# Kernel tuning notes

Measured on AMD Instinct MI355X. Metric: run time of the kernel, lower is better.

The kernel has to match this reference:

```python
import jax, jax.numpy as jnp
import numpy as np

V, D, NH, L, HID, E, K = 32000, 1024, 16, 2, 2048, 8, 2
B, S = 2, 1024
HD = D // NH
EPS = 1e-6
ROPE_BASE = 10000.0


def setup_inputs() -> dict:
    key = jax.random.key(0)
    ks = jax.random.split(key, 12)
    s = 0.02
    return {
        "tokens": jax.random.randint(ks[0], (B, S), 0, V),
        "embed": jax.random.normal(ks[1], (V, D), jnp.float32) * s,
        "attn_norm_w": jnp.ones((L, D), jnp.float32),
        "wq": jax.random.normal(ks[2], (L, D, D), jnp.float32) * s,
        "wk": jax.random.normal(ks[3], (L, D, D), jnp.float32) * s,
        "wv": jax.random.normal(ks[4], (L, D, D), jnp.float32) * s,
        "wo": jax.random.normal(ks[5], (L, D, D), jnp.float32) * s,
        "moe_norm_w": jnp.ones((L, D), jnp.float32),
        "router_w": jax.random.normal(ks[6], (L, E, D), jnp.float32) * s,
        "w1": jax.random.normal(ks[7], (L, E, D, HID), jnp.float32) * s,
        "w2": jax.random.normal(ks[8], (L, E, HID, D), jnp.float32) * s,
        "w3": jax.random.normal(ks[9], (L, E, D, HID), jnp.float32) * s,
        "final_norm_w": jnp.ones((D,), jnp.float32),
    }


def rmsnorm(x, w):
    var = jnp.mean(jnp.square(x), axis=-1, keepdims=True)
    return x * jax.lax.rsqrt(var + EPS) * w


def rope(x):  # x: [B, S, NH, HD], rotate-half convention
    half = HD // 2
    inv = ROPE_BASE ** (-jnp.arange(half, dtype=jnp.float32) / half)
    ang = jnp.arange(x.shape[1], dtype=jnp.float32)[:, None] * inv[None, :]  # [S, half]
    cos = jnp.cos(ang)[None, :, None, :]
    sin = jnp.sin(ang)[None, :, None, :]
    x1, x2 = x[..., :half], x[..., half:]
    return jnp.concatenate([x1 * cos - x2 * sin, x1 * sin + x2 * cos], axis=-1)


def attention(x, wq, wk, wv, wo):
    q = (x @ wq).reshape(B, S, NH, HD)
    k = (x @ wk).reshape(B, S, NH, HD)
    v = (x @ wv).reshape(B, S, NH, HD)
    q, k = rope(q), rope(k)
    scores = jnp.einsum("bqhd,bkhd->bhqk", q, k) / jnp.sqrt(jnp.float32(HD))
    mask = jnp.tril(jnp.ones((S, S), bool))
    scores = jnp.where(mask[None, None], scores, jnp.finfo(scores.dtype).min)
    attn = jax.nn.softmax(scores, axis=-1)
    ctx = jnp.einsum("bhqk,bkhd->bqhd", attn, v).reshape(B, S, D)
    return ctx @ wo


def moe(x, router_w, w1, w2, w3):
    flat = x.reshape(-1, D)                      # [T, D]
    T = flat.shape[0]
    logits = flat @ router_w.T                   # [T, E]
    topv, topi = jax.lax.top_k(logits, K)
    topw = jax.nn.softmax(topv, axis=-1)         # softmax over selected logits
    gates = jnp.zeros((T, E), flat.dtype).at[jnp.arange(T)[:, None], topi].set(topw)
    out = jnp.zeros_like(flat)
    for e in range(E):  # small fixed expert count; gates are exact-sparse so math == dispatch path
        y = (jax.nn.silu(flat @ w1[e]) * (flat @ w3[e])) @ w2[e]
        out = out + y * gates[:, e:e + 1]
    return out.reshape(x.shape)


def reference(tokens, embed, attn_norm_w, wq, wk, wv, wo, moe_norm_w,
              router_w, w1, w2, w3, final_norm_w):
    x = embed[tokens]  # [B, S, D]
    for l in range(L):
        x = x + attention(rmsnorm(x, attn_norm_w[l]), wq[l], wk[l], wv[l], wo[l])
        x = x + moe(rmsnorm(x, moe_norm_w[l]), router_w[l], w1[l], w2[l], w3[l])
    x = rmsnorm(x, final_norm_w)
    return x @ embed.T  # tied logits [B, S, V]
```

## Files before the change

kernel.cpp:

```cpp
#include <hip/hip_runtime.h>
#include <math.h>

typedef unsigned short u16;
typedef unsigned int u32;
typedef __attribute__((ext_vector_type(8))) short bf16x8;
typedef __attribute__((ext_vector_type(4))) float f32x4;

#define TOK 2048
#define SEQ 1024
#define DM 1024
#define NEXP 8
#define VOCAB 32000
#define NL 2
#define SLOTS 5120
#define APAD 40

__device__ __forceinline__ float bf2f(u16 v) {
  u32 u = ((u32)v) << 16; float f; __builtin_memcpy(&f, &u, 4); return f;
}
__device__ __forceinline__ u16 f2bf(float f) {
  u32 u; __builtin_memcpy(&u, &f, 4);
  u += 0x7fffu + ((u >> 16) & 1u);
  return (u16)(u >> 16);
}
// ... 45 lines not shown
  ((ushort4*)(ohi + (long)t * DM))[threadIdx.x] = hi;
  ((ushort4*)(olo + (long)t * DM))[threadIdx.x] = lo;
}

__global__ __launch_bounds__(256) void k_rmsnorm_b(const float* __restrict__ x,
    const float* __restrict__ w, u16* __restrict__ out) {
  int t = blockIdx.x;
  float4 v = ((const float4*)(x + (long)t * DM))[threadIdx.x];
  float ss = v.x * v.x + v.y * v.y + v.z * v.z + v.w * v.w;
  for (int off = 32; off; off >>= 1) ss += __shfl_xor(ss, off);
  __shared__ float red[4];
  if ((threadIdx.x & 63) == 0) red[threadIdx.x >> 6] = ss;
  __syncthreads();
  float tot = red[0] + red[1] + red[2] + red[3];
  float sc = rsqrtf(tot * (1.0f / 1024.0f) + 1e-6f);
  float4 wv = ((const float4*)w)[threadIdx.x];
  ushort4 o;
  o.x = f2bf(v.x * sc * wv.x); o.y = f2bf(v.y * sc * wv.y);
  o.z = f2bf(v.z * sc * wv.z); o.w = f2bf(v.w * sc * wv.w);
  ((ushort4*)(out + (long)t * DM))[threadIdx.x] = o;
}

#define KP 72
#define VP 40
#define PP 36
__global__ __launch_bounds__(256) void k_attn(const float* __restrict__ qkv,
    u16* __restrict__ chi, u16* __restrict__ clo) {
  __shared__ u16 Ksh[32 * KP], Ksl[32 * KP];
  __shared__ u16 Vsh[64 * VP], Vsl[64 * VP];
  __shared__ float Ps[4][16 * PP];
  int bid = blockIdx.x;
  int xcd = bid & 7, r = bid >> 3;
  int bh = xcd * 4 + (r >> 4);
  int qt = r & 15;
  int b = bh >> 4, h = bh & 15;
  int tid = threadIdx.x, w = tid >> 6, lane = tid & 63;
  int lrow = lane & 15, lgrp = lane >> 4;
  int q0 = qt * 64;
  long qrow = (long)(b * SEQ + q0 + w * 16 + lrow);
  bf16x8 qh[2], ql[2];
#pragma unroll
  for (int dsl = 0; dsl < 2; dsl++) {
    const float* src = qkv + qrow * 3072 + h * 64 + dsl * 32 + lgrp * 8;
    float v[8];
    *(float4*)v = *(const float4*)src;
    *(float4*)(v + 4) = *(const float4*)(src + 4);
    u16 hi[8], lo[8];
    split8(v, hi, lo);
    qh[dsl] = *(bf16x8*)hi; ql[dsl] = *(bf16x8*)lo;
  }
  f32x4 cacc[4] = {};
  float mst[4], lst[4];
#pragma unroll
  for (int j = 0; j < 4; j++) { mst[j] = -__builtin_inff(); lst[j] = 0.0f; }
  int srow = tid >> 3, dchunk = (tid & 7) * 8;
  for (int s0 = 0; s0 < q0 + 64; s0 += 32) {
    long kvrow = (long)(b * SEQ + s0 + srow) * 3072 + h * 64;
    {
      const float* ksrc = qkv + kvrow + 1024 + dchunk;
      float v[8];
      *(float4*)v = *(const float4*)ksrc;
      *(float4*)(v + 4) = *(const float4*)(ksrc + 4);
#pragma unroll
      for (int j = 0; j < 8; j++) {
        u16 hi = f2bf(v[j]);
        Ksh[srow * KP + dchunk + j] = hi;
        Ksl[srow * KP + dchunk + j] = f2bf(v[j] - bf2f(hi));
      }
      const float* vsrc = qkv + kvrow + 2048 + dchunk;
      *(float4*)v = *(const float4*)vsrc;
      *(float4*)(v + 4) = *(const float4*)(vsrc + 4);
#pragma unroll
      for (int j = 0; j < 8; j++) {
        u16 hi = f2bf(v[j]);
        Vsh[(dchunk + j) * VP + srow] = hi;
        Vsl[(dchunk + j) * VP + srow] = f2bf(v[j] - bf2f(hi));
      }
    }
    __syncthreads();
    f32x4 sacc[2] = {};
#pragma unroll
    for (int sf = 0; sf < 2; sf++)
#pragma unroll
      for (int dsl = 0; dsl < 2; dsl++) {
        bf16x8 kh = *(const bf16x8*)(Ksh + (sf * 16 + lrow) * KP + dsl * 32 + lgrp * 8);
        bf16x8 kl = *(const bf16x8*)(Ksl + (sf * 16 + lrow) * KP + dsl * 32 + lgrp * 8);
        sacc[sf] = __builtin_amdgcn_mfma_f32_16x16x32_bf16(qh[dsl], kh, sacc[sf], 0, 0, 0);
        sacc[sf] = __builtin_amdgcn_mfma_f32_16x16x32_bf16(qh[dsl], kl, sacc[sf], 0, 0, 0);
        sacc[sf] = __builtin_amdgcn_mfma_f32_16x16x32_bf16(ql[dsl], kh, sacc[sf], 0, 0, 0);
      }
#pragma unroll
    for (int sf = 0; sf < 2; sf++)
#pragma unroll
      for (int j = 0; j < 4; j++) {
        int col = s0 + sf * 16 + lrow;
        int row = q0 + w * 16 + lgrp * 4 + j;
        float v = sacc[sf][j] * 0.125f;
        sacc[sf][j] = (col <= row) ? v : -1e30f;
      }
    float fac[4];
#pragma unroll
    for (int j = 0; j < 4; j++) {
      float mx = fmaxf(sacc[0][j], sacc[1][j]);
      for (int off = 1; off < 16; off <<= 1) mx = fmaxf(mx, __shfl_xor(mx, off));
      float mnew = fmaxf(mst[j], mx);
      float f = __expf(mst[j] - mnew);
      mst[j] = mnew;
      float p0 = __expf(sacc[0][j] - mnew);
      float p1 = __expf(sacc[1][j] - mnew);
      sacc[0][j] = p0; sacc[1][j] = p1;
      float ps = p0 + p1;
      for (int off = 1; off < 16; off <<= 1) ps += __shfl_xor(ps, off);
      lst[j] = lst[j] * f + ps;
      fac[j] = f;
    }
#pragma unroll
    for (int n = 0; n < 4; n++)
#pragma unroll
      for (int j = 0; j < 4; j++) cacc[n][j] *= fac[j];
#pragma unroll
    for (int sf = 0; sf < 2; sf++)
#pragma unroll
      for (int j = 0; j < 4; j++)
        Ps[w][(lgrp * 4 + j) * PP + sf * 16 + lrow] = sacc[sf][j];
    float pv[8];
#pragma unroll
    for (int j = 0; j < 8; j++) pv[j] = Ps[w][lrow * PP + lgrp * 8 + j];
    u16 phi[8], plo[8];
    split8(pv, phi, plo);
    bf16x8 ph = *(bf16x8*)phi, pl = *(bf16x8*)plo;
#pragma unroll
    for (int n = 0; n < 4; n++) {
      bf16x8 vh = *(const bf16x8*)(Vsh + (n * 16 + lrow) * VP + lgrp * 8);
      bf16x8 vl = *(const bf16x8*)(Vsl + (n * 16 + lrow) * VP + lgrp * 8);
      cacc[n] = __builtin_amdgcn_mfma_f32_16x16x32_bf16(ph, vh, cacc[n], 0, 0, 0);
      cacc[n] = __builtin_amdgcn_mfma_f32_16x16x32_bf16(ph, vl, cacc[n], 0, 0, 0);
      cacc[n] = __builtin_amdgcn_mfma_f32_16x16x32_bf16(pl, vh, cacc[n], 0, 0, 0);
    }
    __syncthreads();
  }
#pragma unroll
  for (int n = 0; n < 4; n++)
#pragma unroll
    for (int j = 0; j < 4; j++) {
      long t = (long)(b * SEQ + q0 + w * 16 + lgrp * 4 + j);
      float v = cacc[n][j] / lst[j];
      u16 hv = f2bf(v);
      chi[t * DM + h * 64 + n * 16 + lrow] = hv;
      clo[t * DM + h * 64 + n * 16 + lrow] = f2bf(v - bf2f(hv));
    }
}


__device__ __forceinline__ void stageB_tr(const float* __restrict__ B, int ldb,
    int k0, int n0, u16* Bh, u16* Bl, int tid, int split) {
#pragma unroll
  for (int ph = 0; ph < 2; ph++) {
    int c = tid + 256 * ph;
    int nr = c & 127;
    int ks = c >> 7;
    const float* src = B + (long)(k0 + ks * 8) * ldb + n0 + nr;
    float v[8];
#pragma unroll
    for (int j = 0; j < 8; j++) v[j] = src[(long)j * ldb];
    u16 hi[8];
#pragma unroll
    for (int j = 0; j < 8; j++) hi[j] = f2bf(v[j]);
    *(uint4*)(Bh + nr * APAD + ks * 8) = *(uint4*)hi;
    if (split) {
      u16 lo[8];
#pragma unroll
      for (int j = 0; j < 8; j++) lo[j] = f2bf(v[j] - bf2f(hi[j]));
      *(uint4*)(Bl + nr * APAD + ks * 8) = *(uint4*)lo;
    }
  }
}

__device__ __forceinline__ void stageA_cp(const u16* __restrict__ Ahi,
    const u16* __restrict__ Alo, long ldk, long m0, int k0,
    u16* Ah, u16* Al, int tid, int split) {
#pragma unroll
  for (int ph = 0; ph < 2; ph++) {
    int c = tid + 256 * ph;
    int row = c >> 2, kc = c & 3;
    long off = (m0 + row) * ldk + k0 + kc * 8;
    *(uint4*)(Ah + row * APAD + kc * 8) = *(const uint4*)(Ahi + off);
    if (split) *(uint4*)(Al + row * APAD + kc * 8) = *(const uint4*)(Alo + off);
  }
}

__global__ __launch_bounds__(256) void k_wo(
    const u16* __restrict__ Ahi, const u16* __restrict__ Alo,
    const float* __restrict__ B, float* __restrict__ C) {
  __shared__ u16 Ah[128 * APAD], Al[128 * APAD], Bh[128 * APAD], Bl[128 * APAD];
  int bid = blockIdx.x;
  int n0 = (bid & 7) * 128;
  int m0 = (bid >> 3) * 128;
  int tid = threadIdx.x, lane = tid & 63, w = tid >> 6;
  int wr = w >> 1, wc = w & 1, lrow = lane & 15, lgrp = lane >> 4;
  f32x4 acc[4][4] = {};
  for (int k0 = 0; k0 < 1024; k0 += 32) {
    stageA_cp(Ahi, Alo, DM, m0, k0, Ah, Al, tid, 1);
    stageB_tr(B, 1024, k0, n0, Bh, Bl, tid, 1);
    __syncthreads();
    bf16x8 ah[4], bh[4], al[4], bl[4];
#pragma unroll
    for (int i = 0; i < 4; i++) {
      ah[i] = *(const bf16x8*)(Ah + (wr * 64 + i * 16 + lrow) * APAD + lgrp * 8);
      al[i] = *(const bf16x8*)(Al + (wr * 64 + i * 16 + lrow) * APAD + lgrp * 8);
      bh[i] = *(const bf16x8*)(Bh + (wc * 64 + i * 16 + lrow) * APAD + lgrp * 8);
      bl[i] = *(const bf16x8*)(Bl + (wc * 64 + i * 16 + lrow) * APAD + lgrp * 8);
    }
#pragma unroll
    for (int i = 0; i < 4; i++)
#pragma unroll
      for (int j = 0; j < 4; j++) {
        acc[i][j] = __builtin_amdgcn_mfma_f32_16x16x32_bf16(ah[i], bh[j], acc[i][j], 0, 0, 0);
        acc[i][j] = __builtin_amdgcn_mfma_f32_16x16x32_bf16(ah[i], bl[j], acc[i][j], 0, 0, 0);
        acc[i][j] = __builtin_amdgcn_mfma_f32_16x16x32_bf16(al[i], bh[j], acc[i][j], 0, 0, 0);
      }
    __syncthreads();
  }
#pragma unroll
  for (int i = 0; i < 4; i++)
#pragma unroll
    for (int j = 0; j < 4; j++) {
      int col = n0 + wc * 64 + j * 16 + lrow;
#pragma unroll
      for (int jj = 0; jj < 4; jj++) {
        int r = m0 + wr * 64 + i * 16 + lgrp * 4 + jj;
        C[(long)r * DM + col] += acc[i][j][jj];
      }
    }
}

__global__ __launch_bounds__(256) void k_gemm_qkv(
    const u16* __restrict__ Ahi, const u16* __restrict__ Alo,
    const float* __restrict__ Bq, const float* __restrict__ Bk,
    const float* __restrict__ Bv, float* __restrict__ C) {
  __shared__ u16 Ah[128 * APAD], Al[128 * APAD], Bh[128 * APAD], Bl[128 * APAD];
  int bid = blockIdx.x;
  int xcd = bid & 7, r = bid >> 3;
  int nb = xcd * 3 + r / 16;
  int m0 = (r & 15) * 128;
  const float* B = (nb < 8) ? Bq : (nb < 16) ? Bk : Bv;
  int bn0 = (nb & 7) * 128;
  int tid = threadIdx.x, lane = tid & 63, w = tid >> 6;
  int wr = w >> 1, wc = w & 1, lrow = lane & 15, lgrp = lane >> 4;
  f32x4 acc[4][4] = {};
  for (int k0 = 0; k0 < 1024; k0 += 32) {
    stageA_cp(Ahi, Alo, DM, m0, k0, Ah, Al, tid, 1);
    stageB_tr(B, 1024, k0, bn0, Bh, Bl, tid, 1);
    __syncthreads();
    bf16x8 ah[4], bh[4], al[4], bl[4];
#pragma unroll
    for (int i = 0; i < 4; i++) {
      ah[i] = *(const bf16x8*)(Ah + (wr * 64 + i * 16 + lrow) * APAD + lgrp * 8);
      al[i] = *(const bf16x8*)(Al + (wr * 64 + i * 16 + lrow) * APAD + lgrp * 8);
      bh[i] = *(const bf16x8*)(Bh + (wc * 64 + i * 16 + lrow) * APAD + lgrp * 8);
      bl[i] = *(const bf16x8*)(Bl + (wc * 64 + i * 16 + lrow) * APAD + lgrp * 8);
    }
#pragma unroll
    for (int i = 0; i < 4; i++)
#pragma unroll
      for (int j = 0; j < 4; j++) {
        acc[i][j] = __builtin_amdgcn_mfma_f32_16x16x32_bf16(ah[i], bh[j], acc[i][j], 0, 0, 0);
        acc[i][j] = __builtin_amdgcn_mfma_f32_16x16x32_bf16(ah[i], bl[j], acc[i][j], 0, 0, 0);
        acc[i][j] = __builtin_amdgcn_mfma_f32_16x16x32_bf16(al[i], bh[j], acc[i][j], 0, 0, 0);
      }
    __syncthreads();
  }
  if (nb < 16) {
    float inv1 = exp2f((float)lrow * (-13.287712379549449f / 32.0f));
    float inv2 = exp2f((float)(lrow + 16) * (-13.287712379549449f / 32.0f));
#pragma unroll
    for (int i = 0; i < 4; i++)
#pragma unroll
      for (int jj = 0; jj < 4; jj++) {
        int rr = m0 + wr * 64 + i * 16 + lgrp * 4 + jj;
        float s = (float)(rr & (SEQ - 1));
        float sn1, cs1, sn2, cs2;
        sincosf(s * inv1, &sn1, &cs1);
        sincosf(s * inv2, &sn2, &cs2);
        float q1 = acc[i][0][jj], q2 = acc[i][2][jj];
        acc[i][0][jj] = q1 * cs1 - q2 * sn1;
        acc[i][2][jj] = q1 * sn1 + q2 * cs1;
        float p1 = acc[i][1][jj], p2 = acc[i][3][jj];
        acc[i][1][jj] = p1 * cs2 - p2 * sn2;
        acc[i][3][jj] = p1 * sn2 + p2 * cs2;
      }
  }
#pragma unroll
  for (int i = 0; i < 4; i++)
#pragma unroll
    for (int j = 0; j < 4; j++) {
      int col = nb * 128 + wc * 64 + j * 16 + lrow;
#pragma unroll
      for (int jj = 0; jj < 4; jj++) {
        int rr = m0 + wr * 64 + i * 16 + lgrp * 4 + jj;
        C[(long)rr * 3072 + col] = acc[i][j][jj];
      }
    }
}

template <int SPLIT>
__global__ __launch_bounds__(256) void k_w13(
    const u16* __restrict__ Ahi, const u16* __restrict__ Alo,
    const float* __restrict__ W1, const float* __restrict__ W3,
    const int* __restrict__ lists, const int* __restrict__ counts,
    const int* __restrict__ aoff,
    float* __restrict__ h13) {
  int bid = blockIdx.x;
  int xcd = bid & 7, r = bid >> 3;
  int nb = xcd * 4 + r / 40;
  int m0 = (r % 40) * 128;
  int e = -1;
#pragma unroll
  for (int i = 0; i < NEXP; i++)
    if (m0 >= aoff[i] && m0 < aoff[i + 1]) e = i;
  if (e < 0) return;
  int lr0 = m0 - aoff[e];
  int Mc = counts[e];
  if (lr0 >= Mc) return;
  const float* B = ((nb < 16) ? W1 : W3) + (size_t)e * 1024 * 2048;
  int bn0 = (nb & 15) * 128;
  const int* lst = lists + e * TOK;
  __shared__ u16 Ah[128 * APAD], Bh[128 * APAD];
  __shared__ u16 Al[SPLIT ? 128 * APAD : 1], Bl[SPLIT ? 128 * APAD : 1];
  int tid = threadIdx.x, lane = tid & 63, w = tid >> 6;
  int wr = w >> 1, wc = w & 1, lrow = lane & 15, lgrp = lane >> 4;
  f32x4 acc[4][4] = {};
  for (int k0 = 0; k0 < 1024; k0 += 32) {
#pragma unroll
    for (int ph = 0; ph < 2; ph++) {
      int c = tid + 256 * ph;
      int row = c >> 2, kc = c & 3;
      uint4 vh = make_uint4(0, 0, 0, 0), vl = make_uint4(0, 0, 0, 0);
      if (lr0 + row < Mc) {
        long off = (long)lst[lr0 + row] * DM + k0 + kc * 8;
        vh = *(const uint4*)(Ahi + off);
        if (SPLIT) vl = *(const uint4*)(Alo + off);
      }
      *(uint4*)(Ah + row * APAD + kc * 8) = vh;
      if (SPLIT) *(uint4*)(Al + row * APAD + kc * 8) = vl;
    }
    stageB_tr(B, 2048, k0, bn0, Bh, Bl, tid, SPLIT);
    __syncthreads();
    bf16x8 ah[4], bh[4];
#pragma unroll
    for (int i = 0; i < 4; i++) {
      ah[i] = *(const bf16x8*)(Ah + (wr * 64 + i * 16 + lrow) * APAD + lgrp * 8);
      bh[i] = *(const bf16x8*)(Bh + (wc * 64 + i * 16 + lrow) * APAD + lgrp * 8);
    }
#pragma unroll
    for (int i = 0; i < 4; i++)
#pragma unroll
      for (int j = 0; j < 4; j++)
        acc[i][j] = __builtin_amdgcn_mfma_f32_16x16x32_bf16(ah[i], bh[j], acc[i][j], 0, 0, 0);
    if (SPLIT) {
      bf16x8 al[4], bl[4];
#pragma unroll
      for (int i = 0; i < 4; i++) {
        al[i] = *(const bf16x8*)(Al + (wr * 64 + i * 16 + lrow) * APAD + lgrp * 8);
        bl[i] = *(const bf16x8*)(Bl + (wc * 64 + i * 16 + lrow) * APAD + lgrp * 8);
      }
#pragma unroll
      for (int i = 0; i < 4; i++)
#pragma unroll
        for (int j = 0; j < 4; j++) {
          acc[i][j] = __builtin_amdgcn_mfma_f32_16x16x32_bf16(ah[i], bl[j], acc[i][j], 0, 0, 0);
          acc[i][j] = __builtin_amdgcn_mfma_f32_16x16x32_bf16(al[i], bh[j], acc[i][j], 0, 0, 0);
        }
    }
    __syncthreads();
  }
#pragma unroll
  for (int i = 0; i < 4; i++)
#pragma unroll
    for (int j = 0; j < 4; j++) {
      int col = nb * 128 + wc * 64 + j * 16 + lrow;
#pragma unroll
      for (int jj = 0; jj < 4; jj++) {
        int rl = wr * 64 + i * 16 + lgrp * 4 + jj;
        if (lr0 + rl >= Mc) continue;
        h13[(long)(m0 + rl) * 4096 + col] = acc[i][j][jj];
      }
    }
}

__global__ __launch_bounds__(256) void k_silu(const float* __restrict__ h13,
    const int* __restrict__ counts, const int* __restrict__ aoff,
    u16* __restrict__ hhi, u16* __restrict__ hlo) {
  int g = blockIdx.x;
  int e = -1;
#pragma unroll
  for (int i = 0; i < NEXP; i++)
    if (g >= aoff[i] && g < aoff[i + 1]) e = i;
  if (e < 0 || g - aoff[e] >= counts[e]) return;
  const float4* a = (const float4*)(h13 + (long)g * 4096);
  const float4* b = (const float4*)(h13 + (long)g * 4096 + 2048);
  for (int c = threadIdx.x; c < 512; c += 256) {
    float4 x1 = a[c], x3 = b[c];
    float o[4];
    o[0] = x1.x / (1.0f + __expf(-x1.x)) * x3.x;
    o[1] = x1.y / (1.0f + __expf(-x1.y)) * x3.y;
    o[2] = x1.z / (1.0f + __expf(-x1.z)) * x3.z;
    o[3] = x1.w / (1.0f + __expf(-x1.w)) * x3.w;
    ushort4 hi, lo;
    hi.x = f2bf(o[0]); lo.x = f2bf(o[0] - bf2f(hi.x));
    hi.y = f2bf(o[1]); lo.y = f2bf(o[1] - bf2f(hi.y));
    hi.z = f2bf(o[2]); lo.z = f2bf(o[2] - bf2f(hi.z));
    hi.w = f2bf(o[3]); lo.w = f2bf(o[3] - bf2f(hi.w));
    ((ushort4*)(hhi + (long)g * 2048))[c] = hi;
    ((ushort4*)(hlo + (long)g * 2048))[c] = lo;
  }
}

template <int SPLIT>
__global__ __launch_bounds__(256) void k_w2(
    const u16* __restrict__ Ahi, const u16* __restrict__ Alo,
    const float* __restrict__ W2,
    const int* __restrict__ counts, const int* __restrict__ aoff,
    float* __restrict__ y) {
  int bid = blockIdx.x;
  int n0 = (bid & 7) * 128;
  int m0 = (bid >> 3) * 128;
  int e = -1;
#pragma unroll
  for (int i = 0; i < NEXP; i++)
    if (m0 >= aoff[i] && m0 < aoff[i + 1]) e = i;
  if (e < 0) return;
  int lr0 = m0 - aoff[e];
  int Mc = counts[e];
  if (lr0 >= Mc) return;
  const float* B = W2 + (size_t)e * 2048 * 1024;
  __shared__ u16 Ah[128 * APAD], Bh[128 * APAD];
  __shared__ u16 Al[SPLIT ? 128 * APAD : 1], Bl[SPLIT ? 128 * APAD : 1];
  int tid = threadIdx.x, lane = tid & 63, w = tid >> 6;
  int wr = w >> 1, wc = w & 1, lrow = lane & 15, lgrp = lane >> 4;
  f32x4 acc[4][4] = {};
  for (int k0 = 0; k0 < 2048; k0 += 32) {
    stageA_cp(Ahi, Alo, 2048, m0, k0, Ah, Al, tid, SPLIT);
    stageB_tr(B, 1024, k0, n0, Bh, Bl, tid, SPLIT);
    __syncthreads();
    bf16x8 ah[4], bh[4];
#pragma unroll
    for (int i = 0; i < 4; i++) {
      ah[i] = *(const bf16x8*)(Ah + (wr * 64 + i * 16 + lrow) * APAD + lgrp * 8);
      bh[i] = *(const bf16x8*)(Bh + (wc * 64 + i * 16 + lrow) * APAD + lgrp * 8);
    }
#pragma unroll
    for (int i = 0; i < 4; i++)
#pragma unroll
      for (int j = 0; j < 4; j++)
        acc[i][j] = __builtin_amdgcn_mfma_f32_16x16x32_bf16(ah[i], bh[j], acc[i][j], 0, 0, 0);
    if (SPLIT) {
      bf16x8 al[4], bl[4];
#pragma unroll
      for (int i = 0; i < 4; i++) {
        al[i] = *(const bf16x8*)(Al + (wr * 64 + i * 16 + lrow) * APAD + lgrp * 8);
        bl[i] = *(const bf16x8*)(Bl + (wc * 64 + i * 16 + lrow) * APAD + lgrp * 8);
      }
#pragma unroll
      for (int i = 0; i < 4; i++)
#pragma unroll
        for (int j = 0; j < 4; j++) {
          acc[i][j] = __builtin_amdgcn_mfma_f32_16x16x32_bf16(ah[i], bl[j], acc[i][j], 0, 0, 0);
          acc[i][j] = __builtin_amdgcn_mfma_f32_16x16x32_bf16(al[i], bh[j], acc[i][j], 0, 0, 0);
        }
    }
    __syncthreads();
  }
#pragma unroll
  for (int i = 0; i < 4; i++)
#pragma unroll
    for (int j = 0; j < 4; j++) {
      int col = n0 + wc * 64 + j * 16 + lrow;
#pragma unroll
      for (int jj = 0; jj < 4; jj++) {
        int rl = wr * 64 + i * 16 + lgrp * 4 + jj;
        if (lr0 + rl >= Mc) continue;
        y[(long)(m0 + rl) * DM + col] = acc[i][j][jj];
      }
    }
}

__global__ __launch_bounds__(256) void k_combine(const float* __restrict__ y,
    const int* __restrict__ aoff, const int* __restrict__ tok_e,
    const int* __restrict__ tok_pos, const float* __restrict__ tok_gate,
    float* __restrict__ x) {
  int t = blockIdx.x;
  float4 acc = ((float4*)(x + (long)t * DM))[threadIdx.x];
#pragma unroll
  for (int j = 0; j < 2; j++) {
    int e = tok_e[t * 2 + j];
    long g = aoff[e] + tok_pos[t * 2 + j];
    float gt = tok_gate[t * 2 + j];
    float4 yv = ((const float4*)(y + g * DM))[threadIdx.x];
    acc.x += gt * yv.x; acc.y += gt * yv.y;
    acc.z += gt * yv.z; acc.w += gt * yv.w;
  }
  ((float4*)(x + (long)t * DM))[threadIdx.x] = acc;
}

__device__ __forceinline__ void logits_mma(const u16* As, const u16* Bs,
    f32x4 (&acc)[4][4], int wr, int wc, int lrow, int lgrp) {
  bf16x8 af[4], bfr[4];
#pragma unroll
  for (int i = 0; i < 4; i++) {
    af[i] = *(const bf16x8*)(As + (wr * 64 + i * 16 + lrow) * APAD + lgrp * 8);
    bfr[i] = *(const bf16x8*)(Bs + (wc * 64 + i * 16 + lrow) * APAD + lgrp * 8);
  }
#pragma unroll
  for (int i = 0; i < 4; i++)
#pragma unroll
    for (int j = 0; j < 4; j++)
      acc[i][j] = __builtin_amdgcn_mfma_f32_16x16x32_bf16(af[i], bfr[j], acc[i][j], 0, 0, 0);
}

__global__ __launch_bounds__(512) void k_logits(
    const u16* __restrict__ A, const u16* __restrict__ Bt,
    float* __restrict__ C) {
  __shared__ u16 AsA[256 * APAD], BsA[128 * APAD];
  __shared__ u16 AsB[256 * APAD], BsB[128 * APAD];
  int bid = blockIdx.x;
  int xcd = bid & 7, rank = bid >> 3;
  int bx = xcd * 32 + (rank >> 3);
  int by = rank & 7;
  if (bx >= VOCAB / 128) return;
  int m0 = by * 256, n0 = bx * 128;
  int tid = threadIdx.x, lane = tid & 63, w = tid >> 6;
  int wr = w >> 1, wc = w & 1;
  int lrow = lane & 15, lgrp = lane >> 4;
  int arow = tid >> 2, akc = tid & 3;
  f32x4 acc[4][4] = {};
  const u16* Ap = A + (long)(m0 + arow) * 1024 + akc * 8;
  const u16* Ap2 = A + (long)(m0 + arow + 128) * 1024 + akc * 8;
  const u16* Bp = Bt + (long)(n0 + arow) * 1024 + akc * 8;
  uint4 a0 = *(const uint4*)(Ap);
  uint4 a1 = *(const uint4*)(Ap2);
  uint4 b0 = *(const uint4*)(Bp);
  *(uint4*)(AsA + arow * APAD + akc * 8) = a0;
  *(uint4*)(AsA + (arow + 128) * APAD + akc * 8) = a1;
  *(uint4*)(BsA + arow * APAD + akc * 8) = b0;
  __syncthreads();
  for (int kt = 0; kt < 32; kt += 2) {
    {
      int k0 = (kt + 1) * 32;
      a0 = *(const uint4*)(Ap + k0);
      a1 = *(const uint4*)(Ap2 + k0);
      b0 = *(const uint4*)(Bp + k0);
    }
    logits_mma(AsA, BsA, acc, wr, wc, lrow, lgrp);
    *(uint4*)(AsB + arow * APAD + akc * 8) = a0;
    *(uint4*)(AsB + (arow + 128) * APAD + akc * 8) = a1;
    *(uint4*)(BsB + arow * APAD + akc * 8) = b0;
    __syncthreads();
    if (kt + 2 < 32) {
      int k0 = (kt + 2) * 32;
      a0 = *(const uint4*)(Ap + k0);
      a1 = *(const uint4*)(Ap2 + k0);
      b0 = *(const uint4*)(Bp + k0);
    }
    logits_mma(AsB, BsB, acc, wr, wc, lrow, lgrp);
    if (kt + 2 < 32) {
      *(uint4*)(AsA + arow * APAD + akc * 8) = a0;
      *(uint4*)(AsA + (arow + 128) * APAD + akc * 8) = a1;
      *(uint4*)(BsA + arow * APAD + akc * 8) = b0;
    }
    __syncthreads();
  }
#pragma unroll
  for (int i = 0; i < 4; i++)
#pragma unroll
    for (int j = 0; j < 4; j++) {
      int col = n0 + wc * 64 + j * 16 + lrow;
#pragma unroll
      for (int jj = 0; jj < 4; jj++) {
        int r = m0 + wr * 64 + i * 16 + lgrp * 4 + jj;
        C[(long)r * VOCAB + col] = acc[i][j][jj];
      }
    }
}

__global__ __launch_bounds__(256) void k_router(const float* __restrict__ x,
    const float* __restrict__ nw, const float* __restrict__ rw,
    int* __restrict__ counts, int* __restrict__ lists,
    int* __restrict__ tok_e, int* __restrict__ tok_pos,
    float* __restrict__ tok_gate) {
  int t = blockIdx.x * 4 + (threadIdx.x >> 6);
  int lane = threadIdx.x & 63;
  const float* xr = x + (long)t * DM;
  float ss = 0.0f;
  float p[8] = {0, 0, 0, 0, 0, 0, 0, 0};
  for (int i = 0; i < 16; i++) {
    int d = lane + 64 * i;
    float xv = xr[d];
    ss += xv * xv;
    float xw = xv * nw[d];
#pragma unroll
    for (int e = 0; e < 8; e++) p[e] += xw * rw[e * DM + d];
  }
  for (int off = 32; off; off >>= 1) ss += __shfl_xor(ss, off);
#pragma unroll
  for (int e = 0; e < 8; e++)
    for (int off = 32; off; off >>= 1) p[e] += __shfl_xor(p[e], off);
  if (lane == 0) {
    float sc = rsqrtf(ss * (1.0f / 1024.0f) + 1e-6f);
    int e0 = 0, e1 = -1;
    float v0 = -__builtin_inff(), v1 = -__builtin_inff();
    for (int e = 0; e < 8; e++) {
      float pe = p[e] * sc;
      if (pe > v0) { v1 = v0; e1 = e0; v0 = pe; e0 = e; }
      else if (pe > v1) { v1 = pe; e1 = e; }
    }
    float w0 = 1.0f / (1.0f + expf(v1 - v0));
    int pos0 = atomicAdd(&counts[e0], 1);
    lists[e0 * TOK + pos0] = t;
    tok_e[t * 2] = e0; tok_pos[t * 2] = pos0; tok_gate[t * 2] = w0;
    int pos1 = atomicAdd(&counts[e1], 1);
    lists[e1 * TOK + pos1] = t;
    tok_e[t * 2 + 1] = e1; tok_pos[t * 2 + 1] = pos1; tok_gate[t * 2 + 1] = 1.0f - w0;
// ... 92 lines not shown
```

Before: 1.459 ms.

## Double-buffer LDS tiles with register prefetch in all GEMM kernels

Converts the wo, qkv, MoE w1/w3 and w2 GEMM main loops to a ping-pong LDS scheme. Each thread loads the next K tile's A and B data from global memory into registers before issuing MFMAs on the current buffer, then writes it to the other buffer. This hides global-load latency behind matrix math and cuts the per-iteration barriers from two to one. It doubles shared memory per block (about 80KB in the split kernels) and raises register pressure, which may reduce occupancy.

```diff
diff --git a/kernel.cpp b/kernel.cpp
--- a/kernel.cpp
+++ b/kernel.cpp
@@ -221,73 +221,128 @@
 }
 
 
-__device__ __forceinline__ void stageB_tr(const float* __restrict__ B, int ldb,
-    int k0, int n0, u16* Bh, u16* Bl, int tid, int split) {
-#pragma unroll
-  for (int ph = 0; ph < 2; ph++) {
-    int c = tid + 256 * ph;
-    int nr = c & 127;
-    int ks = c >> 7;
-    const float* src = B + (long)(k0 + ks * 8) * ldb + n0 + nr;
-    float v[8];
-#pragma unroll
-    for (int j = 0; j < 8; j++) v[j] = src[(long)j * ldb];
-    u16 hi[8];
-#pragma unroll
-    for (int j = 0; j < 8; j++) hi[j] = f2bf(v[j]);
-    *(uint4*)(Bh + nr * APAD + ks * 8) = *(uint4*)hi;
-    if (split) {
-      u16 lo[8];
-#pragma unroll
-      for (int j = 0; j < 8; j++) lo[j] = f2bf(v[j] - bf2f(hi[j]));
-      *(uint4*)(Bl + nr * APAD + ks * 8) = *(uint4*)lo;
-    }
-  }
-}
-
-__device__ __forceinline__ void stageA_cp(const u16* __restrict__ Ahi,
-    const u16* __restrict__ Alo, long ldk, long m0, int k0,
-    u16* Ah, u16* Al, int tid, int split) {
-#pragma unroll
-  for (int ph = 0; ph < 2; ph++) {
-    int c = tid + 256 * ph;
-    int row = c >> 2, kc = c & 3;
-    long off = (m0 + row) * ldk + k0 + kc * 8;
-    *(uint4*)(Ah + row * APAD + kc * 8) = *(const uint4*)(Ahi + off);
-    if (split) *(uint4*)(Al + row * APAD + kc * 8) = *(const uint4*)(Alo + off);
+__device__ __forceinline__ void mma1(const u16* Ah, const u16* Bh,
+    f32x4 (&acc)[4][4], int wr, int wc, int lrow, int lgrp) {
+  bf16x8 ah[4], bh[4];
+#pragma unroll
+  for (int i = 0; i < 4; i++) {
+    ah[i] = *(const bf16x8*)(Ah + (wr * 64 + i * 16 + lrow) * APAD + lgrp * 8);
+    bh[i] = *(const bf16x8*)(Bh + (wc * 64 + i * 16 + lrow) * APAD + lgrp * 8);
+  }
+#pragma unroll
+  for (int i = 0; i < 4; i++)
+#pragma unroll
+    for (int j = 0; j < 4; j++)
+      acc[i][j] = __builtin_amdgcn_mfma_f32_16x16x32_bf16(ah[i], bh[j], acc[i][j], 0, 0, 0);
+}
+
+__device__ __forceinline__ void mma3(const u16* Ah, const u16* Al,
+    const u16* Bh, const u16* Bl, f32x4 (&acc)[4][4],
+    int wr, int wc, int lrow, int lgrp) {
+  bf16x8 ah[4], bh[4], al[4], bl[4];
+#pragma unroll
+  for (int i = 0; i < 4; i++) {
+    ah[i] = *(const bf16x8*)(Ah + (wr * 64 + i * 16 + lrow) * APAD + lgrp * 8);
+    al[i] = *(const bf16x8*)(Al + (wr * 64 + i * 16 + lrow) * APAD + lgrp * 8);
+    bh[i] = *(const bf16x8*)(Bh + (wc * 64 + i * 16 + lrow) * APAD + lgrp * 8);
+    bl[i] = *(const bf16x8*)(Bl + (wc * 64 + i * 16 + lrow) * APAD + lgrp * 8);
+  }
+#pragma unroll
+  for (int i = 0; i < 4; i++)
+#pragma unroll
+    for (int j = 0; j < 4; j++) {
+      acc[i][j] = __builtin_amdgcn_mfma_f32_16x16x32_bf16(ah[i], bh[j], acc[i][j], 0, 0, 0);
+      acc[i][j] = __builtin_amdgcn_mfma_f32_16x16x32_bf16(ah[i], bl[j], acc[i][j], 0, 0, 0);
+      acc[i][j] = __builtin_amdgcn_mfma_f32_16x16x32_bf16(al[i], bh[j], acc[i][j], 0, 0, 0);
+    }
+}
+
+__device__ __forceinline__ void wrA(u16* Ah, u16* Al, int arow, int akc,
+    uint4 h1, uint4 l1, uint4 h2, uint4 l2, int split) {
+  *(uint4*)(Ah + arow * APAD + akc * 8) = h1;
+  *(uint4*)(Ah + (arow + 64) * APAD + akc * 8) = h2;
+  if (split) {
+    *(uint4*)(Al + arow * APAD + akc * 8) = l1;
+    *(uint4*)(Al + (arow + 64) * APAD + akc * 8) = l2;
+  }
+}
+__device__ __forceinline__ void wrB(u16* Bh, u16* Bl, int bnr, int bks,
+    const float* v1, const float* v2, int split) {
+  u16 hi[8];
+#pragma unroll
+  for (int j = 0; j < 8; j++) hi[j] = f2bf(v1[j]);
+  *(uint4*)(Bh + bnr * APAD + bks * 8) = *(uint4*)hi;
+  if (split) {
+    u16 lo[8];
+#pragma unroll
+    for (int j = 0; j < 8; j++) lo[j] = f2bf(v1[j] - bf2f(hi[j]));
+    *(uint4*)(Bl + bnr * APAD + bks * 8) = *(uint4*)lo;
+  }
+#pragma unroll
+  for (int j = 0; j < 8; j++) hi[j] = f2bf(v2[j]);
+  *(uint4*)(Bh + bnr * APAD + (bks + 2) * 8) = *(uint4*)hi;
+  if (split) {
+    u16 lo[8];
+#pragma unroll
+    for (int j = 0; j < 8; j++) lo[j] = f2bf(v2[j] - bf2f(hi[j]));
+    *(uint4*)(Bl + bnr * APAD + (bks + 2) * 8) = *(uint4*)lo;
   }
 }
 
 __global__ __launch_bounds__(256) void k_wo(
     const u16* __restrict__ Ahi, const u16* __restrict__ Alo,
     const float* __restrict__ B, float* __restrict__ C) {
-  __shared__ u16 Ah[128 * APAD], Al[128 * APAD], Bh[128 * APAD], Bl[128 * APAD];
+  __shared__ u16 AhA[128 * APAD], AlA[128 * APAD], BhA[128 * APAD], BlA[128 * APAD];
+  __shared__ u16 AhB[128 * APAD], AlB[128 * APAD], BhB[128 * APAD], BlB[128 * APAD];
   int bid = blockIdx.x;
   int n0 = (bid & 7) * 128;
   int m0 = (bid >> 3) * 128;
   int tid = threadIdx.x, lane = tid & 63, w = tid >> 6;
   int wr = w >> 1, wc = w & 1, lrow = lane & 15, lgrp = lane >> 4;
+  int arow = tid >> 2, akc = tid & 3;
+  int bnr = tid & 127, bks = tid >> 7;
+  const u16* pAh = Ahi + (long)(m0 + arow) * DM + akc * 8;
+  const u16* pAl = Alo + (long)(m0 + arow) * DM + akc * 8;
+  const float* pB1 = B + (long)(bks * 8) * 1024 + n0 + bnr;
+  const float* pB2 = B + (long)((bks + 2) * 8) * 1024 + n0 + bnr;
+  uint4 h1, l1, h2, l2;
+  float b1[8], b2[8];
   f32x4 acc[4][4] = {};
-  for (int k0 = 0; k0 < 1024; k0 += 32) {
-    stageA_cp(Ahi, Alo, DM, m0, k0, Ah, Al, tid, 1);
-    stageB_tr(B, 1024, k0, n0, Bh, Bl, tid, 1);
-    __syncthreads();
-    bf16x8 ah[4], bh[4], al[4], bl[4];
-#pragma unroll
-    for (int i = 0; i < 4; i++) {
-      ah[i] = *(const bf16x8*)(Ah + (wr * 64 + i * 16 + lrow) * APAD + lgrp * 8);
-      al[i] = *(const bf16x8*)(Al + (wr * 64 + i * 16 + lrow) * APAD + lgrp * 8);
-      bh[i] = *(const bf16x8*)(Bh + (wc * 64 + i * 16 + lrow) * APAD + lgrp * 8);
-      bl[i] = *(const bf16x8*)(Bl + (wc * 64 + i * 16 + lrow) * APAD + lgrp * 8);
-    }
-#pragma unroll
-    for (int i = 0; i < 4; i++)
-#pragma unroll
-      for (int j = 0; j < 4; j++) {
-        acc[i][j] = __builtin_amdgcn_mfma_f32_16x16x32_bf16(ah[i], bh[j], acc[i][j], 0, 0, 0);
-        acc[i][j] = __builtin_amdgcn_mfma_f32_16x16x32_bf16(ah[i], bl[j], acc[i][j], 0, 0, 0);
-        acc[i][j] = __builtin_amdgcn_mfma_f32_16x16x32_bf16(al[i], bh[j], acc[i][j], 0, 0, 0);
-      }
+  h1 = *(const uint4*)(pAh); l1 = *(const uint4*)(pAl);
+  h2 = *(const uint4*)(pAh + 64 * DM); l2 = *(const uint4*)(pAl + 64 * DM);
+#pragma unroll
+  for (int j = 0; j < 8; j++) { b1[j] = pB1[(long)j * 1024]; b2[j] = pB2[(long)j * 1024]; }
+  wrA(AhA, AlA, arow, akc, h1, l1, h2, l2, 1);
+  wrB(BhA, BlA, bnr, bks, b1, b2, 1);
+  __syncthreads();
+  for (int kt = 0; kt < 32; kt += 2) {
+    {
+      int k0 = (kt + 1) * 32;
+      h1 = *(const uint4*)(pAh + k0); l1 = *(const uint4*)(pAl + k0);
+      h2 = *(const uint4*)(pAh + 64 * DM + k0); l2 = *(const uint4*)(pAl + 64 * DM + k0);
+      const float* q1 = pB1 + (long)k0 * 1024;
+      const float* q2 = pB2 + (long)k0 * 1024;
+#pragma unroll
+      for (int j = 0; j < 8; j++) { b1[j] = q1[(long)j * 1024]; b2[j] = q2[(long)j * 1024]; }
+    }
+    mma3(AhA, AlA, BhA, BlA, acc, wr, wc, lrow, lgrp);
+    wrA(AhB, AlB, arow, akc, h1, l1, h2, l2, 1);
+    wrB(BhB, BlB, bnr, bks, b1, b2, 1);
+    __syncthreads();
+    if (kt + 2 < 32) {
+      int k0 = (kt + 2) * 32;
+      h1 = *(const uint4*)(pAh + k0); l1 = *(const uint4*)(pAl + k0);
+      h2 = *(const uint4*)(pAh + 64 * DM + k0); l2 = *(const uint4*)(pAl + 64 * DM + k0);
+      const float* q1 = pB1 + (long)k0 * 1024;
+      const float* q2 = pB2 + (long)k0 * 1024;
+#pragma unroll
+      for (int j = 0; j < 8; j++) { b1[j] = q1[(long)j * 1024]; b2[j] = q2[(long)j * 1024]; }
+    }
+    mma3(AhB, AlB, BhB, BlB, acc, wr, wc, lrow, lgrp);
+    if (kt + 2 < 32) {
+      wrA(AhA, AlA, arow, akc, h1, l1, h2, l2, 1);
+      wrB(BhA, BlA, bnr, bks, b1, b2, 1);
+    }
     __syncthreads();
   }
 #pragma unroll
@@ -307,7 +362,8 @@
     const u16* __restrict__ Ahi, const u16* __restrict__ Alo,
     const float* __restrict__ Bq, const float* __restrict__ Bk,
     const float* __restrict__ Bv, float* __restrict__ C) {
-  __shared__ u16 Ah[128 * APAD], Al[128 * APAD], Bh[128 * APAD], Bl[128 * APAD];
+  __shared__ u16 AhA[128 * APAD], AlA[128 * APAD], BhA[128 * APAD], BlA[128 * APAD];
+  __shared__ u16 AhB[128 * APAD], AlB[128 * APAD], BhB[128 * APAD], BlB[128 * APAD];
   int bid = blockIdx.x;
   int xcd = bid & 7, r = bid >> 3;
   int nb = xcd * 3 + r / 16;
@@ -316,27 +372,50 @@
   int bn0 = (nb & 7) * 128;
   int tid = threadIdx.x, lane = tid & 63, w = tid >> 6;
   int wr = w >> 1, wc = w & 1, lrow = lane & 15, lgrp = lane >> 4;
+  int arow = tid >> 2, akc = tid & 3;
+  int bnr = tid & 127, bks = tid >> 7;
+  const u16* pAh = Ahi + (long)(m0 + arow) * DM + akc * 8;
+  const u16* pAl = Alo + (long)(m0 + arow) * DM + akc * 8;
+  const float* pB1 = B + (long)(bks * 8) * 1024 + bn0 + bnr;
+  const float* pB2 = B + (long)((bks + 2) * 8) * 1024 + bn0 + bnr;
+  uint4 h1, l1, h2, l2;
+  float b1[8], b2[8];
   f32x4 acc[4][4] = {};
-  for (int k0 = 0; k0 < 1024; k0 += 32) {
-    stageA_cp(Ahi, Alo, DM, m0, k0, Ah, Al, tid, 1);
-    stageB_tr(B, 1024, k0, bn0, Bh, Bl, tid, 1);
-    __syncthreads();
-    bf16x8 ah[4], bh[4], al[4], bl[4];
-#pragma unroll
-    for (int i = 0; i < 4; i++) {
-      ah[i] = *(const bf16x8*)(Ah + (wr * 64 + i * 16 + lrow) * APAD + lgrp * 8);
-      al[i] = *(const bf16x8*)(Al + (wr * 64 + i * 16 + lrow) * APAD + lgrp * 8);
-      bh[i] = *(const bf16x8*)(Bh + (wc * 64 + i * 16 + lrow) * APAD + lgrp * 8);
-      bl[i] = *(const bf16x8*)(Bl + (wc * 64 + i * 16 + lrow) * APAD + lgrp * 8);
-    }
-#pragma unroll
-    for (int i = 0; i < 4; i++)
-#pragma unroll
-      for (int j = 0; j < 4; j++) {
-        acc[i][j] = __builtin_amdgcn_mfma_f32_16x16x32_bf16(ah[i], bh[j], acc[i][j], 0, 0, 0);
-        acc[i][j] = __builtin_amdgcn_mfma_f32_16x16x32_bf16(ah[i], bl[j], acc[i][j], 0, 0, 0);
-        acc[i][j] = __builtin_amdgcn_mfma_f32_16x16x32_bf16(al[i], bh[j], acc[i][j], 0, 0, 0);
-      }
+  h1 = *(const uint4*)(pAh); l1 = *(const uint4*)(pAl);
+  h2 = *(const uint4*)(pAh + 64 * DM); l2 = *(const uint4*)(pAl + 64 * DM);
+#pragma unroll
+  for (int j = 0; j < 8; j++) { b1[j] = pB1[(long)j * 1024]; b2[j] = pB2[(long)j * 1024]; }
+  wrA(AhA, AlA, arow, akc, h1, l1, h2, l2, 1);
+  wrB(BhA, BlA, bnr, bks, b1, b2, 1);
+  __syncthreads();
+  for (int kt = 0; kt < 32; kt += 2) {
+    {
+      int k0 = (kt + 1) * 32;
+      h1 = *(const uint4*)(pAh + k0); l1 = *(const uint4*)(pAl + k0);
+      h2 = *(const uint4*)(pAh + 64 * DM + k0); l2 = *(const uint4*)(pAl + 64 * DM + k0);
+      const float* q1 = pB1 + (long)k0 * 1024;
+      const float* q2 = pB2 + (long)k0 * 1024;
+#pragma unroll
+      for (int j = 0; j < 8; j++) { b1[j] = q1[(long)j * 1024]; b2[j] = q2[(long)j * 1024]; }
+    }
+    mma3(AhA, AlA, BhA, BlA, acc, wr, wc, lrow, lgrp);
+    wrA(AhB, AlB, arow, akc, h1, l1, h2, l2, 1);
+    wrB(BhB, BlB, bnr, bks, b1, b2, 1);
+    __syncthreads();
+    if (kt + 2 < 32) {
+      int k0 = (kt + 2) * 32;
+      h1 = *(const uint4*)(pAh + k0); l1 = *(const uint4*)(pAl + k0);
+      h2 = *(const uint4*)(pAh + 64 * DM + k0); l2 = *(const uint4*)(pAl + 64 * DM + k0);
+      const float* q1 = pB1 + (long)k0 * 1024;
+      const float* q2 = pB2 + (long)k0 * 1024;
+#pragma unroll
+      for (int j = 0; j < 8; j++) { b1[j] = q1[(long)j * 1024]; b2[j] = q2[(long)j * 1024]; }
+    }
+    mma3(AhB, AlB, BhB, BlB, acc, wr, wc, lrow, lgrp);
+    if (kt + 2 < 32) {
+      wrA(AhA, AlA, arow, akc, h1, l1, h2, l2, 1);
+      wrB(BhA, BlA, bnr, bks, b1, b2, 1);
+    }
     __syncthreads();
   }
   if (nb < 16) {
@@ -394,52 +473,68 @@
   const float* B = ((nb < 16) ? W1 : W3) + (size_t)e * 1024 * 2048;
   int bn0 = (nb & 15) * 128;
   const int* lst = lists + e * TOK;
-  __shared__ u16 Ah[128 * APAD], Bh[128 * APAD];
-  __shared__ u16 Al[SPLIT ? 128 * APAD : 1], Bl[SPLIT ? 128 * APAD : 1];
+  __shared__ u16 AhA[128 * APAD], BhA[128 * APAD];
+  __shared__ u16 AhB[128 * APAD], BhB[128 * APAD];
+  __shared__ u16 AlA[SPLIT ? 128 * APAD : 1], BlA[SPLIT ? 128 * APAD : 1];
+  __shared__ u16 AlB[SPLIT ? 128 * APAD : 1], BlB[SPLIT ? 128 * APAD : 1];
   int tid = threadIdx.x, lane = tid & 63, w = tid >> 6;
   int wr = w >> 1, wc = w & 1, lrow = lane & 15, lgrp = lane >> 4;
+  int arow = tid >> 2, akc = tid & 3;
+  int bnr = tid & 127, bks = tid >> 7;
+  long g1 = (lr0 + arow < Mc) ? (long)lst[lr0 + arow] : -1;
+  long g2 = (lr0 + arow + 64 < Mc) ? (long)lst[lr0 + arow + 64] : -1;
+  const u16* pAh1 = (g1 >= 0) ? Ahi + g1 * DM + akc * 8 : nullptr;
+  const u16* pAl1 = (g1 >= 0) ? Alo + g1 * DM + akc * 8 : nullptr;
+  const u16* pAh2 = (g2 >= 0) ? Ahi + g2 * DM + akc * 8 : nullptr;
+  const u16* pAl2 = (g2 >= 0) ? Alo + g2 * DM + akc * 8 : nullptr;
+  const float* pB1 = B + (long)(bks * 8) * 2048 + bn0 + bnr;
+  const float* pB2 = B + (long)((bks + 2) * 8) * 2048 + bn0 + bnr;
+  uint4 h1, l1, h2, l2;
+  float b1[8], b2[8];
   f32x4 acc[4][4] = {};
-  for (int k0 = 0; k0 < 1024; k0 += 32) {
-#pragma unroll
-    for (int ph = 0; ph < 2; ph++) {
-      int c = tid + 256 * ph;
-      int row = c >> 2, kc = c & 3;
-      uint4 vh = make_uint4(0, 0, 0, 0), vl = make_uint4(0, 0, 0, 0);
-      if (lr0 + row < Mc) {
-        long off = (long)lst[lr0 + row] * DM + k0 + kc * 8;
-        vh = *(const uint4*)(Ahi + off);
-        if (SPLIT) vl = *(const uint4*)(Alo + off);
-      }
-      *(uint4*)(Ah + row * APAD + kc * 8) = vh;
-      if (SPLIT) *(uint4*)(Al + row * APAD + kc * 8) = vl;
-    }
-    stageB_tr(B, 2048, k0, bn0, Bh, Bl, tid, SPLIT);
-    __syncthreads();
-    bf16x8 ah[4], bh[4];
-#pragma unroll
-    for (int i = 0; i < 4; i++) {
-      ah[i] = *(const bf16x8*)(Ah + (wr * 64 + i * 16 + lrow) * APAD + lgrp * 8);
-      bh[i] = *(const bf16x8*)(Bh + (wc * 64 + i * 16 + lrow) * APAD + lgrp * 8);
-    }
-#pragma unroll
-    for (int i = 0; i < 4; i++)
-#pragma unroll
-      for (int j = 0; j < 4; j++)
-        acc[i][j] = __builtin_amdgcn_mfma_f32_16x16x32_bf16(ah[i], bh[j], acc[i][j], 0, 0, 0);
-    if (SPLIT) {
-      bf16x8 al[4], bl[4];
-#pragma unroll
-      for (int i = 0; i < 4; i++) {
-        al[i] = *(const bf16x8*)(Al + (wr * 64 + i * 16 + lrow) * APAD + lgrp * 8);
-        bl[i] = *(const bf16x8*)(Bl + (wc * 64 + i * 16 + lrow) * APAD + lgrp * 8);
-      }
-#pragma unroll
-      for (int i = 0; i < 4; i++)
-#pragma unroll
-        for (int j = 0; j < 4; j++) {
-          acc[i][j] = __builtin_amdgcn_mfma_f32_16x16x32_bf16(ah[i], bl[j], acc[i][j], 0, 0, 0);
-          acc[i][j] = __builtin_amdgcn_mfma_f32_16x16x32_bf16(al[i], bh[j], acc[i][j], 0, 0, 0);
-        }
+  uint4 z = make_uint4(0, 0, 0, 0);
+  h1 = (g1 >= 0) ? *(const uint4*)(pAh1) : z;
+  h2 = (g2 >= 0) ? *(const uint4*)(pAh2) : z;
+  l1 = (SPLIT && g1 >= 0) ? *(const uint4*)(pAl1) : z;
+  l2 = (SPLIT && g2 >= 0) ? *(const uint4*)(pAl2) : z;
+#pragma unroll
+  for (int j = 0; j < 8; j++) { b1[j] = pB1[(long)j * 2048]; b2[j] = pB2[(long)j * 2048]; }
+  wrA(AhA, AlA, arow, akc, h1, l1, h2, l2, SPLIT);
+  wrB(BhA, BlA, bnr, bks, b1, b2, SPLIT);
+  __syncthreads();
+  for (int kt = 0; kt < 32; kt += 2) {
+    {
+      int k0 = (kt + 1) * 32;
+      h1 = (g1 >= 0) ? *(const uint4*)(pAh1 + k0) : z;
+      h2 = (g2 >= 0) ? *(const uint4*)(pAh2 + k0) : z;
+      l1 = (SPLIT && g1 >= 0) ? *(const uint4*)(pAl1 + k0) : z;
+      l2 = (SPLIT && g2 >= 0) ? *(const uint4*)(pAl2 + k0) : z;
+      const float* q1 = pB1 + (long)k0 * 2048;
+      const float* q2 = pB2 + (long)k0 * 2048;
+#pragma unroll
+      for (int j = 0; j < 8; j++) { b1[j] = q1[(long)j * 2048]; b2[j] = q2[(long)j * 2048]; }
+    }
+    if (SPLIT) mma3(AhA, AlA, BhA, BlA, acc, wr, wc, lrow, lgrp);
+    else mma1(AhA, BhA, acc, wr, wc, lrow, lgrp);
+    wrA(AhB, AlB, arow, akc, h1, l1, h2, l2, SPLIT);
+    wrB(BhB, BlB, bnr, bks, b1, b2, SPLIT);
+    __syncthreads();
+    if (kt + 2 < 32) {
+      int k0 = (kt + 2) * 32;
+      h1 = (g1 >= 0) ? *(const uint4*)(pAh1 + k0) : z;
+      h2 = (g2 >= 0) ? *(const uint4*)(pAh2 + k0) : z;
+      l1 = (SPLIT && g1 >= 0) ? *(const uint4*)(pAl1 + k0) : z;
+      l2 = (SPLIT && g2 >= 0) ? *(const uint4*)(pAl2 + k0) : z;
+      const float* q1 = pB1 + (long)k0 * 2048;
+      const float* q2 = pB2 + (long)k0 * 2048;
+#pragma unroll
+      for (int j = 0; j < 8; j++) { b1[j] = q1[(long)j * 2048]; b2[j] = q2[(long)j * 2048]; }
+    }
+    if (SPLIT) mma3(AhB, AlB, BhB, BlB, acc, wr, wc, lrow, lgrp);
+    else mma1(AhB, BhB, acc, wr, wc, lrow, lgrp);
+    if (kt + 2 < 32) {
+      wrA(AhA, AlA, arow, akc, h1, l1, h2, l2, SPLIT);
+      wrB(BhA, BlA, bnr, bks, b1, b2, SPLIT);
     }
     __syncthreads();
   }
@@ -503,40 +598,62 @@
   int Mc = counts[e];
   if (lr0 >= Mc) return;
   const float* B = W2 + (size_t)e * 2048 * 1024;
-  __shared__ u16 Ah[128 * APAD], Bh[128 * APAD];
-  __shared__ u16 Al[SPLIT ? 128 * APAD : 1], Bl[SPLIT ? 128 * APAD : 1];
+  __shared__ u16 AhA[128 * APAD], BhA[128 * APAD];
+  __shared__ u16 AhB[128 * APAD], BhB[128 * APAD];
+  __shared__ u16 AlA[SPLIT ? 128 * APAD : 1], BlA[SPLIT ? 128 * APAD : 1];
+  __shared__ u16 AlB[SPLIT ? 128 * APAD : 1], BlB[SPLIT ? 128 * APAD : 1];
   int tid = threadIdx.x, lane = tid & 63, w = tid >> 6;
   int wr = w >> 1, wc = w & 1, lrow = lane & 15, lgrp = lane >> 4;
+  int arow = tid >> 2, akc = tid & 3;
+  int bnr = tid & 127, bks = tid >> 7;
+  const u16* pAh = Ahi + (long)(m0 + arow) * 2048 + akc * 8;
+  const u16* pAl = Alo + (long)(m0 + arow) * 2048 + akc * 8;
+  const float* pB1 = B + (long)(bks * 8) * 1024 + n0 + bnr;
+  const float* pB2 = B + (long)((bks + 2) * 8) * 1024 + n0 + bnr;
+  uint4 h1, l1, h2, l2;
+  float b1[8], b2[8];
   f32x4 acc[4][4] = {};
-  for (int k0 = 0; k0 < 2048; k0 += 32) {
-    stageA_cp(Ahi, Alo, 2048, m0, k0, Ah, Al, tid, SPLIT);
-    stageB_tr(B, 1024, k0, n0, Bh, Bl, tid, SPLIT);
-    __syncthreads();
-    bf16x8 ah[4], bh[4];
-#pragma unroll
-    for (int i = 0; i < 4; i++) {
-      ah[i] = *(const bf16x8*)(Ah + (wr * 64 + i * 16 + lrow) * APAD + lgrp * 8);
-      bh[i] = *(const bf16x8*)(Bh + (wc * 64 + i * 16 + lrow) * APAD + lgrp * 8);
-    }
-#pragma unroll
-    for (int i = 0; i < 4; i++)
-#pragma unroll
-      for (int j = 0; j < 4; j++)
-        acc[i][j] = __builtin_amdgcn_mfma_f32_16x16x32_bf16(ah[i], bh[j], acc[i][j], 0, 0, 0);
-    if (SPLIT) {
-      bf16x8 al[4], bl[4];
-#pragma unroll
-      for (int i = 0; i < 4; i++) {
-        al[i] = *(const bf16x8*)(Al + (wr * 64 + i * 16 + lrow) * APAD + lgrp * 8);
-        bl[i] = *(const bf16x8*)(Bl + (wc * 64 + i * 16 + lrow) * APAD + lgrp * 8);
-      }
-#pragma unroll
-      for (int i = 0; i < 4; i++)
-#pragma unroll
-        for (int j = 0; j < 4; j++) {
-          acc[i][j] = __builtin_amdgcn_mfma_f32_16x16x32_bf16(ah[i], bl[j], acc[i][j], 0, 0, 0);
-          acc[i][j] = __builtin_amdgcn_mfma_f32_16x16x32_bf16(al[i], bh[j], acc[i][j], 0, 0, 0);
-        }
+  uint4 z = make_uint4(0, 0, 0, 0);
+  h1 = *(const uint4*)(pAh);
+  h2 = *(const uint4*)(pAh + 64 * 2048);
+  l1 = SPLIT ? *(const uint4*)(pAl) : z;
+  l2 = SPLIT ? *(const uint4*)(pAl + 64 * 2048) : z;
+#pragma unroll
+  for (int j = 0; j < 8; j++) { b1[j] = pB1[(long)j * 1024]; b2[j] = pB2[(long)j * 1024]; }
+  wrA(AhA, AlA, arow, akc, h1, l1, h2, l2, SPLIT);
+  wrB(BhA, BlA, bnr, bks, b1, b2, SPLIT);
+  __syncthreads();
+  for (int kt = 0; kt < 64; kt += 2) {
+    {
+      int k0 = (kt + 1) * 32;
+      h1 = *(const uint4*)(pAh + k0);
+      h2 = *(const uint4*)(pAh + 64 * 2048 + k0);
+      if (SPLIT) { l1 = *(const uint4*)(pAl + k0); l2 = *(const uint4*)(pAl + 64 * 2048 + k0); }
+      const float* q1 = pB1 + (long)k0 * 1024;
+      const float* q2 = pB2 + (long)k0 * 1024;
+#pragma unroll
+      for (int j = 0; j < 8; j++) { b1[j] = q1[(long)j * 1024]; b2[j] = q2[(long)j * 1024]; }
+    }
+    if (SPLIT) mma3(AhA, AlA, BhA, BlA, acc, wr, wc, lrow, lgrp);
+    else mma1(AhA, BhA, acc, wr, wc, lrow, lgrp);
+    wrA(AhB, AlB, arow, akc, h1, l1, h2, l2, SPLIT);
+    wrB(BhB, BlB, bnr, bks, b1, b2, SPLIT);
+    __syncthreads();
+    if (kt + 2 < 64) {
+      int k0 = (kt + 2) * 32;
+      h1 = *(const uint4*)(pAh + k0);
+      h2 = *(const uint4*)(pAh + 64 * 2048 + k0);
+      if (SPLIT) { l1 = *(const uint4*)(pAl + k0); l2 = *(const uint4*)(pAl + 64 * 2048 + k0); }
+      const float* q1 = pB1 + (long)k0 * 1024;
+      const float* q2 = pB2 + (long)k0 * 1024;
+#pragma unroll
+      for (int j = 0; j < 8; j++) { b1[j] = q1[(long)j * 1024]; b2[j] = q2[(long)j * 1024]; }
+    }
+    if (SPLIT) mma3(AhB, AlB, BhB, BlB, acc, wr, wc, lrow, lgrp);
+    else mma1(AhB, BhB, acc, wr, wc, lrow, lgrp);
+    if (kt + 2 < 64) {
+      wrA(AhA, AlA, arow, akc, h1, l1, h2, l2, SPLIT);
+      wrB(BhA, BlA, bnr, bks, b1, b2, SPLIT);
     }
     __syncthreads();
   }
```

Measured after the change: 1.698 ms. +16.3%, slower.
